# Performance work log

Hardware: AMD Instinct MI355X
Metric: run time of the kernel (lower is better)

Reference implementation:

```python
import jax, jax.numpy as jnp
import numpy as np

N_NODES = 100000
N_EDGES = 1600000
D_IN = 256
D_OUT = 128


def setup_inputs() -> dict:
    key = jax.random.key(0)
    k1, k2, k3, k4, k5, k6 = jax.random.split(key, 6)
    inp = {
        "input": jax.random.normal(k1, (N_NODES, D_IN), dtype=jnp.float32),
        "edge_row": jax.random.randint(k2, (N_EDGES,), 0, N_NODES),
        "edge_col": jax.random.randint(k3, (N_EDGES,), 0, N_NODES),
        "edge_val": jax.random.uniform(k4, (N_EDGES,), dtype=jnp.float32),
        "W": jax.random.normal(k5, (D_IN, D_OUT), dtype=jnp.float32) * (1.0 / np.sqrt(D_IN)),
        "b": jax.random.normal(k6, (D_OUT,), dtype=jnp.float32) * 0.01,
    }
    return inp


def reference(input, edge_row, edge_col, edge_val, W, b):
    # support = Linear(input)  -> [N, D_OUT]
    support = jnp.dot(input, W) + b
    # sparse.mm(adj, support): out[r] = sum_e val[e] * support[col[e]] for edges with row[e]==r
    msgs = edge_val[:, None] * support[edge_col]  # [E, D_OUT]
    agg = jax.ops.segment_sum(msgs, edge_row, num_segments=N_NODES)  # [N, D_OUT]
    return jnp.tanh(agg)
```

## Files before the change

kernel.cpp:

```cpp
#include <hip/hip_runtime.h>
#include <math.h>

#define N_NODES 100000
#define N_EDGES 1600000
#define D_IN 256
#define D_OUT 128

#define OFF_SUPPORT 0
#define OFF_COUNTS  51200000
#define OFF_CSREV   51600008
#define OFF_BSUMS   64400008
#define OFF_WTHI    64400416
#define OFF_WTLO    64465952

#define SCAN_CHUNK  1024
#define SCAN_BLOCKS ((N_NODES + SCAN_CHUNK - 1) / SCAN_CHUNK)

#define GB 128
#define GEMM_BLOCKS ((N_NODES + GB - 1) / GB)
#define EDGE_BLOCKS ((N_EDGES + 255) / 256)
#define WCONV_BLOCKS ((D_IN * D_OUT) / 256)

typedef __attribute__((ext_vector_type(8))) short s8v;
typedef __attribute__((ext_vector_type(4))) float f4v;

__device__ __forceinline__ short f2bf(float x) {
  unsigned u = __float_as_uint(x);
  unsigned r = u + 0x7FFF + ((u >> 16) & 1);
  return (short)(r >> 16);
}
__device__ __forceinline__ float bf2f(short h) {
  return __uint_as_float(((unsigned)(unsigned short)h) << 16);
}

__device__ __forceinline__ void cvt8(float4 a, float4 b, s8v& h, s8v& l) {
  float f[8] = {a.x, a.y, a.z, a.w, b.x, b.y, b.z, b.w};
#pragma unroll
  for (int i = 0; i < 8; i++) {
    short hh = f2bf(f[i]);
    h[i] = hh;
    l[i] = f2bf(f[i] - bf2f(hh));
  }
}

__device__ __forceinline__ void gload_lds16(const void* g, void* l) {
  __builtin_amdgcn_global_load_lds(
      (const __attribute__((address_space(1))) void*)g,
      (__attribute__((address_space(3))) void*)l, 16, 0, 0);
}

#define VMW(N)                                             \
  asm volatile("s_waitcnt vmcnt(" #N ")" ::: "memory");    \
  __builtin_amdgcn_sched_barrier(0)
#define SBAR()                    \
  __builtin_amdgcn_s_barrier();   \
  __builtin_amdgcn_sched_barrier(0)

__global__ __launch_bounds__(256) void prep_kernel(
    const float* __restrict__ W, short* __restrict__ wt_hi,
    short* __restrict__ wt_lo, const int* __restrict__ erow,
    int* __restrict__ counts, int* __restrict__ pos_e) {
  if (blockIdx.x < WCONV_BLOCKS) {
    int idx = blockIdx.x * 256 + threadIdx.x;
    int k = idx >> 7;
    int n = idx & 127;
    float v = W[idx];
    short h = f2bf(v);
    wt_hi[n * 256 + k] = h;
    wt_lo[n * 256 + k] = f2bf(v - bf2f(h));
  } else {
    int e = (blockIdx.x - WCONV_BLOCKS) * 256 + threadIdx.x;
    if (e < N_EDGES) pos_e[e] = atomicAdd(&counts[erow[e]], 1);
  }
}

__device__ __forceinline__ void gemm_body(
    int gb, const float* __restrict__ input, const short* __restrict__ wt_hi,
    const short* __restrict__ wt_lo, const float* __restrict__ b,
    float* __restrict__ support) {
  __shared__ short Bh[2][128][64];
  __shared__ short Bl[2][128][64];
  const int t = threadIdx.x;
  const int lane = t & 63;
  const int wv = t >> 6;
  const int qm = lane & 15;
  const int quad = lane >> 4;
  const int node0 = gb * GB;

  int r0 = node0 + wv * 32 + qm;
  int r1 = r0 + 16;
  if (r0 > N_NODES - 1) r0 = N_NODES - 1;
  if (r1 > N_NODES - 1) r1 = N_NODES - 1;
  const float* a0p = input + (size_t)r0 * D_IN + quad * 8;
  const float* a1p = input + (size_t)r1 * D_IN + quad * 8;

  const int lrow = lane >> 3;
  const int lpc = lane & 7;
  auto stageB = [&](int q, int p) {
    const int rb = wv * 32;
#pragma unroll
    for (int j = 0; j < 4; ++j) {
      int n = rb + j * 8 + lrow;
      int sc = lpc ^ (n & 7);
      const short* sh = wt_hi + (size_t)n * 256 + q * 64 + sc * 8;
      const short* sl = wt_lo + (size_t)n * 256 + q * 64 + sc * 8;
      gload_lds16(sh, &Bh[p][rb + j * 8][0]);
      gload_lds16(sl, &Bl[p][rb + j * 8][0]);
    }
  };

  float4 A0[4], A1[4], A2[4];
  auto loadA = [&](float4* d, int s) {
    d[0] = *(const float4*)(a0p + s * 32);
    d[1] = *(const float4*)(a0p + s * 32 + 4);
    d[2] = *(const float4*)(a1p + s * 32);
    d[3] = *(const float4*)(a1p + s * 32 + 4);
  };

  f4v acc[2][8];
#pragma unroll
  for (int mt = 0; mt < 2; mt++)
#pragma unroll
    for (int nt = 0; nt < 8; nt++) acc[mt][nt] = (f4v){0.f, 0.f, 0.f, 0.f};

  s8v ah0, al0, ah1, al1;
  auto cvtA = [&](const float4* X) {
    cvt8(X[0], X[1], ah0, al0);
    cvt8(X[2], X[3], ah1, al1);
  };
  auto mfma8 = [&](int p, int si) {
#pragma unroll
    for (int nt = 0; nt < 8; ++nt) {
      int n = nt * 16 + qm;
      int pc = (si * 4 + quad) ^ (n & 7);
      s8v bh = *(const s8v*)&Bh[p][n][pc * 8];
      s8v bl = *(const s8v*)&Bl[p][n][pc * 8];
      acc[0][nt] = __builtin_amdgcn_mfma_f32_16x16x32_bf16(ah0, bh, acc[0][nt], 0, 0, 0);
      acc[0][nt] = __builtin_amdgcn_mfma_f32_16x16x32_bf16(ah0, bl, acc[0][nt], 0, 0, 0);
      acc[0][nt] = __builtin_amdgcn_mfma_f32_16x16x32_bf16(al0, bh, acc[0][nt], 0, 0, 0);
      acc[1][nt] = __builtin_amdgcn_mfma_f32_16x16x32_bf16(ah1, bh, acc[1][nt], 0, 0, 0);
      acc[1][nt] = __builtin_amdgcn_mfma_f32_16x16x32_bf16(ah1, bl, acc[1][nt], 0, 0, 0);
      acc[1][nt] = __builtin_amdgcn_mfma_f32_16x16x32_bf16(al1, bh, acc[1][nt], 0, 0, 0);
    }
  };

  stageB(0, 0);
  loadA(A0, 0);
  loadA(A1, 1);
  loadA(A2, 2);
  VMW(8);
  SBAR();
  cvtA(A0);
  stageB(1, 1);
  loadA(A0, 3);
  mfma8(0, 0);
  VMW(16);
  cvtA(A1);
  loadA(A1, 4);
  mfma8(0, 1);
  VMW(8);
  SBAR();
  cvtA(A2);
  stageB(2, 0);
  loadA(A2, 5);
  mfma8(1, 0);
  VMW(16);
  cvtA(A0);
  loadA(A0, 6);
  mfma8(1, 1);
  VMW(8);
  SBAR();
  cvtA(A1);
  stageB(3, 1);
  loadA(A1, 7);
  mfma8(0, 0);
  VMW(16);
  cvtA(A2);
  mfma8(0, 1);
  VMW(4);
  SBAR();
  cvtA(A0);
  mfma8(1, 0);
  VMW(0);
  cvtA(A1);
  mfma8(1, 1);

  float bias[8];
#pragma unroll
  for (int nt = 0; nt < 8; nt++) bias[nt] = b[nt * 16 + qm];
#pragma unroll
  for (int mt = 0; mt < 2; mt++) {
#pragma unroll
    for (int nt = 0; nt < 8; nt++) {
      int col = nt * 16 + qm;
#pragma unroll
      for (int r = 0; r < 4; r++) {
        int node = node0 + wv * 32 + mt * 16 + quad * 4 + r;
        if (node < N_NODES)
          support[(size_t)node * D_OUT + col] = acc[mt][nt][r] + bias[nt];
      }
    }
  }
}

__global__ __launch_bounds__(256, 2) void gemm_build_kernel(
    const float* __restrict__ input, const short* __restrict__ wt_hi,
    const short* __restrict__ wt_lo, const float* __restrict__ b,
    float* __restrict__ support, const int* __restrict__ erow,
    const int* __restrict__ ecol, const float* __restrict__ eval,
    const int* __restrict__ offsets, const int* __restrict__ pos_e,
    long long* __restrict__ csr_ev) {
  if (blockIdx.x < GEMM_BLOCKS) {
    gemm_body(blockIdx.x, input, wt_hi, wt_lo, b, support);
  } else {
    int e = (blockIdx.x - GEMM_BLOCKS) * 256 + threadIdx.x;
    if (e < N_EDGES) {
      int r = __builtin_nontemporal_load(erow + e);
      int c = __builtin_nontemporal_load(ecol + e);
      int vb = __builtin_nontemporal_load((const int*)eval + e);
      int p = __builtin_nontemporal_load(pos_e + e);
      int idx = offsets[r] + p;
      long long packed = (unsigned int)c | ((long long)(unsigned int)vb << 32);
      csr_ev[idx] = packed;
    }
  }
}

__global__ __launch_bounds__(256) void scan_phase1(const int* __restrict__ counts,
                                                   int* __restrict__ bsums) {
  __shared__ int ts[256];
  int t = threadIdx.x;
  int idx0 = blockIdx.x * SCAN_CHUNK + t * 4;
  int s = 0;
#pragma unroll
  for (int i = 0; i < 4; i++)
    if (idx0 + i < N_NODES) s += counts[idx0 + i];
  ts[t] = s;
  __syncthreads();
#pragma unroll
  for (int off = 128; off > 0; off >>= 1) {
    if (t < off) ts[t] += ts[t + off];
    __syncthreads();
  }
  if (t == 0) bsums[blockIdx.x] = ts[0];
}

__global__ __launch_bounds__(128) void scan_phase2(int* __restrict__ bsums) {
  __shared__ int s[128];
  int t = threadIdx.x;
  int v = (t < SCAN_BLOCKS) ? bsums[t] : 0;
  s[t] = v;
  __syncthreads();
#pragma unroll
  for (int off = 1; off < 128; off <<= 1) {
    int x = (t >= off) ? s[t - off] : 0;
    __syncthreads();
    s[t] += x;
    __syncthreads();
  }
  if (t < SCAN_BLOCKS) bsums[t] = s[t] - v;
}

__global__ __launch_bounds__(256) void scan_phase3(int* __restrict__ counts,
                                                   const int* __restrict__ bsums) {
  __shared__ int ts[256];
  int t = threadIdx.x;
  int b = blockIdx.x;
  int idx0 = b * SCAN_CHUNK + t * 4;
  int v[4];
  int s = 0;
#pragma unroll
  for (int i = 0; i < 4; i++) {
    v[i] = (idx0 + i < N_NODES) ? counts[idx0 + i] : 0;
    s += v[i];
  }
  ts[t] = s;
  __syncthreads();
#pragma unroll
  for (int off = 1; off < 256; off <<= 1) {
    int x = (t >= off) ? ts[t - off] : 0;
    __syncthreads();
    ts[t] += x;
    __syncthreads();
  }
  int run = bsums[b] + ts[t] - s;
#pragma unroll
  for (int i = 0; i < 4; i++) {
    int idx = idx0 + i;
    if (idx < N_NODES) counts[idx] = run;
    run += v[i];
  }
  if (b == 0 && t == 0) counts[N_NODES] = N_EDGES;
}

__global__ __launch_bounds__(256) void agg_kernel(
    const int* __restrict__ offsets, const long long* __restrict__ csr_ev,
    const float* __restrict__ support, float* __restrict__ out) {
  int r = blockIdx.x * 8 + (threadIdx.x >> 5);
  int l4 = (threadIdx.x & 31) * 4;
  int beg = offsets[r];
  int end = offsets[r + 1];
  float4 acc = make_float4(0.f, 0.f, 0.f, 0.f);

  if (end > beg) {
    int ec[8], encol[8];
    float ev[8], env[8];
#pragma unroll
    for (int u = 0; u < 8; u++) {
      int idx = beg + u;
      int c = idx < end ? idx : end - 1;
      long long p = csr_ev[c];
      ec[u] = (int)(unsigned int)p;
      ev[u] = (idx < end) ? __uint_as_float((unsigned int)(p >> 32)) : 0.f;
    }
    for (int j = beg; j < end; j += 8) {
      int jn = j + 8;
      if (jn < end) {
#pragma unroll
        for (int u = 0; u < 8; u++) {
          int idx = jn + u;
          int c = idx < end ? idx : end - 1;
          long long p = csr_ev[c];
          encol[u] = (int)(unsigned int)p;
          env[u] = (idx < end) ? __uint_as_float((unsigned int)(p >> 32)) : 0.f;
        }
      }
      float4 s[8];
#pragma unroll
      for (int u = 0; u < 8; u++)
        s[u] = *(const float4*)(support + (size_t)ec[u] * D_OUT + l4);
#pragma unroll
      for (int u = 0; u < 8; u++) {
        acc.x = fmaf(ev[u], s[u].x, acc.x);
        acc.y = fmaf(ev[u], s[u].y, acc.y);
        acc.z = fmaf(ev[u], s[u].z, acc.z);
        acc.w = fmaf(ev[u], s[u].w, acc.w);
      }
#pragma unroll
      for (int u = 0; u < 8; u++) { ec[u] = encol[u]; ev[u] = env[u]; }
    }
  }
  *(float4*)(out + (size_t)r * D_OUT + l4) =
      make_float4(tanhf(acc.x), tanhf(acc.y), tanhf(acc.z), tanhf(acc.w));
}

extern "C" void kernel_launch(void* const* d_in, const int* in_sizes, int n_in,
                              void* d_out, int out_size, void* d_ws, size_t ws_size,
                              hipStream_t stream) {
  const float* input = (const float*)d_in[0];
  const int* erow = (const int*)d_in[1];
  const int* ecol = (const int*)d_in[2];
  const float* eval = (const float*)d_in[3];
  const float* W = (const float*)d_in[4];
  const float* b = (const float*)d_in[5];
  float* out = (float*)d_out;

  char* ws = (char*)d_ws;
  float* support = (float*)(ws + OFF_SUPPORT);
  int* counts = (int*)(ws + OFF_COUNTS);
  long long* csr_ev = (long long*)(ws + OFF_CSREV);
  int* bsums = (int*)(ws + OFF_BSUMS);
  short* wt_hi = (short*)(ws + OFF_WTHI);
  short* wt_lo = (short*)(ws + OFF_WTLO);
  int* pos_e = (int*)d_out;

  hipMemsetAsync(ws + OFF_COUNTS, 0, (size_t)(N_NODES + 1) * 4, stream);

  hipLaunchKernelGGL(prep_kernel, dim3(WCONV_BLOCKS + EDGE_BLOCKS), dim3(256),
                     0, stream, W, wt_hi, wt_lo, erow, counts, pos_e);
  hipLaunchKernelGGL(scan_phase1, dim3(SCAN_BLOCKS), dim3(256), 0, stream,
                     counts, bsums);
  hipLaunchKernelGGL(scan_phase2, dim3(1), dim3(128), 0, stream, bsums);
  hipLaunchKernelGGL(scan_phase3, dim3(SCAN_BLOCKS), dim3(256), 0, stream,
                     counts, bsums);
  hipLaunchKernelGGL(gemm_build_kernel, dim3(GEMM_BLOCKS + EDGE_BLOCKS),
                     dim3(256), 0, stream, input, wt_hi, wt_lo, b, support,
                     erow, ecol, eval, counts, pos_e, csr_ev);
  hipLaunchKernelGGL(agg_kernel, dim3(N_NODES / 8), dim3(256), 0, stream,
                     counts, csr_ev, support, out);
}
```

Before: 422.7 us.

## Replace three-phase scan with single-pass decoupled lookback scan and batch edge work

Merges the three scan kernels into one decoupled-lookback scan that publishes per-block aggregate and inclusive flags in a state array, which prep_kernel zeroes. This removes two kernel launches and the dependency gaps between them. The histogram and CSR-build edge blocks now process 8 edges per thread with loads batched ahead of atomics and scatters, to expose more memory-level parallelism. The lookback spin-waits on earlier blocks and relies on all 98 scan blocks making forward progress.

```diff
diff --git a/kernel.cpp b/kernel.cpp
--- a/kernel.cpp
+++ b/kernel.cpp
@@ -9,7 +9,7 @@
 #define OFF_SUPPORT 0
 #define OFF_COUNTS  51200000
 #define OFF_CSREV   51600008
-#define OFF_BSUMS   64400008
+#define OFF_STATE   64400008
 #define OFF_WTHI    64400416
 #define OFF_WTLO    64465952
 
@@ -18,8 +18,9 @@
 
 #define GB 128
 #define GEMM_BLOCKS ((N_NODES + GB - 1) / GB)
-#define EDGE_BLOCKS ((N_EDGES + 255) / 256)
 #define WCONV_BLOCKS ((D_IN * D_OUT) / 256)
+#define HIST_BLOCKS ((N_EDGES + 2047) / 2048)
+#define BUILD_BLOCKS ((N_EDGES + 2047) / 2048)
 
 typedef __attribute__((ext_vector_type(8))) short s8v;
 typedef __attribute__((ext_vector_type(4))) float f4v;
@@ -59,19 +60,94 @@
 __global__ __launch_bounds__(256) void prep_kernel(
     const float* __restrict__ W, short* __restrict__ wt_hi,
     short* __restrict__ wt_lo, const int* __restrict__ erow,
-    int* __restrict__ counts, int* __restrict__ pos_e) {
+    int* __restrict__ counts, int* __restrict__ pos_e,
+    unsigned* __restrict__ state) {
+  const int t = threadIdx.x;
   if (blockIdx.x < WCONV_BLOCKS) {
-    int idx = blockIdx.x * 256 + threadIdx.x;
+    int idx = blockIdx.x * 256 + t;
     int k = idx >> 7;
     int n = idx & 127;
     float v = W[idx];
     short h = f2bf(v);
     wt_hi[n * 256 + k] = h;
     wt_lo[n * 256 + k] = f2bf(v - bf2f(h));
+    if (blockIdx.x == 0 && t < SCAN_BLOCKS) state[t] = 0;
   } else {
-    int e = (blockIdx.x - WCONV_BLOCKS) * 256 + threadIdx.x;
-    if (e < N_EDGES) pos_e[e] = atomicAdd(&counts[erow[e]], 1);
-  }
+    int base = (blockIdx.x - WCONV_BLOCKS) * 2048 + t;
+    int r[8];
+#pragma unroll
+    for (int u = 0; u < 8; u++) {
+      int e = base + u * 256;
+      r[u] = (e < N_EDGES) ? erow[e] : -1;
+    }
+#pragma unroll
+    for (int u = 0; u < 8; u++) {
+      int e = base + u * 256;
+      if (r[u] >= 0) pos_e[e] = atomicAdd(&counts[r[u]], 1);
+    }
+  }
+}
+
+__global__ __launch_bounds__(256) void scan_kernel(
+    int* __restrict__ counts, unsigned* __restrict__ state) {
+  __shared__ int ts[256];
+  __shared__ int sprev;
+  const int t = threadIdx.x;
+  const int b = blockIdx.x;
+  int idx0 = b * SCAN_CHUNK + t * 4;
+  int v[4];
+  int s = 0;
+#pragma unroll
+  for (int i = 0; i < 4; i++) {
+    v[i] = (idx0 + i < N_NODES) ? counts[idx0 + i] : 0;
+    s += v[i];
+  }
+  ts[t] = s;
+  __syncthreads();
+#pragma unroll
+  for (int off = 1; off < 256; off <<= 1) {
+    int x = (t >= off) ? ts[t - off] : 0;
+    __syncthreads();
+    ts[t] += x;
+    __syncthreads();
+  }
+  int total = ts[255];
+  if (t == 0)
+    atomicExch(&state[b], ((unsigned)total << 2) | (b == 0 ? 2u : 1u));
+  if (b == 0) {
+    if (t == 0) sprev = 0;
+  } else if (t < 64) {
+    unsigned run = 0;
+    int look = b - 1;
+    for (;;) {
+      int p = look - t;
+      unsigned sv = 2u;
+      if (p >= 0) {
+        do { sv = atomicAdd(&state[p], 0u); } while ((sv & 3u) == 0u);
+      }
+      unsigned long long mask = __ballot((sv & 3u) == 2u);
+      int fl = (mask != 0ULL) ? (__ffsll((long long)mask) - 1) : 64;
+      unsigned c = (t <= fl) ? (sv >> 2) : 0u;
+#pragma unroll
+      for (int o = 32; o > 0; o >>= 1) c += __shfl_down(c, o);
+      if (t == 0) run += c;
+      if (mask != 0ULL) break;
+      look -= 64;
+    }
+    if (t == 0) {
+      sprev = (int)run;
+      atomicExch(&state[b], ((run + (unsigned)total) << 2) | 2u);
+    }
+  }
+  __syncthreads();
+  int run0 = sprev + ts[t] - s;
+#pragma unroll
+  for (int i = 0; i < 4; i++) {
+    int idx = idx0 + i;
+    if (idx < N_NODES) counts[idx] = run0;
+    run0 += v[i];
+  }
+  if (b == 0 && t == 0) counts[N_NODES] = N_EDGES;
 }
 
 __device__ __forceinline__ void gemm_body(
@@ -213,84 +289,32 @@
   if (blockIdx.x < GEMM_BLOCKS) {
     gemm_body(blockIdx.x, input, wt_hi, wt_lo, b, support);
   } else {
-    int e = (blockIdx.x - GEMM_BLOCKS) * 256 + threadIdx.x;
-    if (e < N_EDGES) {
-      int r = __builtin_nontemporal_load(erow + e);
-      int c = __builtin_nontemporal_load(ecol + e);
-      int vb = __builtin_nontemporal_load((const int*)eval + e);
-      int p = __builtin_nontemporal_load(pos_e + e);
-      int idx = offsets[r] + p;
-      long long packed = (unsigned int)c | ((long long)(unsigned int)vb << 32);
-      csr_ev[idx] = packed;
-    }
-  }
-}
-
-__global__ __launch_bounds__(256) void scan_phase1(const int* __restrict__ counts,
-                                                   int* __restrict__ bsums) {
-  __shared__ int ts[256];
-  int t = threadIdx.x;
-  int idx0 = blockIdx.x * SCAN_CHUNK + t * 4;
-  int s = 0;
-#pragma unroll
-  for (int i = 0; i < 4; i++)
-    if (idx0 + i < N_NODES) s += counts[idx0 + i];
-  ts[t] = s;
-  __syncthreads();
-#pragma unroll
-  for (int off = 128; off > 0; off >>= 1) {
-    if (t < off) ts[t] += ts[t + off];
-    __syncthreads();
-  }
-  if (t == 0) bsums[blockIdx.x] = ts[0];
-}
-
-__global__ __launch_bounds__(128) void scan_phase2(int* __restrict__ bsums) {
-  __shared__ int s[128];
-  int t = threadIdx.x;
-  int v = (t < SCAN_BLOCKS) ? bsums[t] : 0;
-  s[t] = v;
-  __syncthreads();
-#pragma unroll
-  for (int off = 1; off < 128; off <<= 1) {
-    int x = (t >= off) ? s[t - off] : 0;
-    __syncthreads();
-    s[t] += x;
-    __syncthreads();
-  }
-  if (t < SCAN_BLOCKS) bsums[t] = s[t] - v;
-}
-
-__global__ __launch_bounds__(256) void scan_phase3(int* __restrict__ counts,
-                                                   const int* __restrict__ bsums) {
-  __shared__ int ts[256];
-  int t = threadIdx.x;
-  int b = blockIdx.x;
-  int idx0 = b * SCAN_CHUNK + t * 4;
-  int v[4];
-  int s = 0;
-#pragma unroll
-  for (int i = 0; i < 4; i++) {
-    v[i] = (idx0 + i < N_NODES) ? counts[idx0 + i] : 0;
-    s += v[i];
-  }
-  ts[t] = s;
-  __syncthreads();
-#pragma unroll
-  for (int off = 1; off < 256; off <<= 1) {
-    int x = (t >= off) ? ts[t - off] : 0;
-    __syncthreads();
-    ts[t] += x;
-    __syncthreads();
-  }
-  int run = bsums[b] + ts[t] - s;
-#pragma unroll
-  for (int i = 0; i < 4; i++) {
-    int idx = idx0 + i;
-    if (idx < N_NODES) counts[idx] = run;
-    run += v[i];
-  }
-  if (b == 0 && t == 0) counts[N_NODES] = N_EDGES;
+    int base = (blockIdx.x - GEMM_BLOCKS) * 2048 + threadIdx.x;
+    int r[8], p[8];
+#pragma unroll
+    for (int u = 0; u < 8; u++) {
+      int e = base + u * 256;
+      bool ok = e < N_EDGES;
+      r[u] = ok ? __builtin_nontemporal_load(erow + e) : -1;
+      p[u] = ok ? __builtin_nontemporal_load(pos_e + e) : 0;
+    }
+    int off[8];
+#pragma unroll
+    for (int u = 0; u < 8; u++) off[u] = (r[u] >= 0) ? offsets[r[u]] : 0;
+    long long pk[8];
+#pragma unroll
+    for (int u = 0; u < 8; u++) {
+      int e = base + u * 256;
+      if (r[u] >= 0) {
+        int c = __builtin_nontemporal_load(ecol + e);
+        int vb = __builtin_nontemporal_load((const int*)eval + e);
+        pk[u] = (unsigned)c | ((long long)(unsigned)vb << 32);
+      }
+    }
+#pragma unroll
+    for (int u = 0; u < 8; u++)
+      if (r[u] >= 0) csr_ev[off[u] + p[u]] = pk[u];
+  }
 }
 
 __global__ __launch_bounds__(256) void agg_kernel(
@@ -359,21 +383,18 @@
   float* support = (float*)(ws + OFF_SUPPORT);
   int* counts = (int*)(ws + OFF_COUNTS);
   long long* csr_ev = (long long*)(ws + OFF_CSREV);
-  int* bsums = (int*)(ws + OFF_BSUMS);
+  unsigned* state = (unsigned*)(ws + OFF_STATE);
   short* wt_hi = (short*)(ws + OFF_WTHI);
   short* wt_lo = (short*)(ws + OFF_WTLO);
   int* pos_e = (int*)d_out;
 
   hipMemsetAsync(ws + OFF_COUNTS, 0, (size_t)(N_NODES + 1) * 4, stream);
 
-  hipLaunchKernelGGL(prep_kernel, dim3(WCONV_BLOCKS + EDGE_BLOCKS), dim3(256),
-                     0, stream, W, wt_hi, wt_lo, erow, counts, pos_e);
-  hipLaunchKernelGGL(scan_phase1, dim3(SCAN_BLOCKS), dim3(256), 0, stream,
-                     counts, bsums);
-  hipLaunchKernelGGL(scan_phase2, dim3(1), dim3(128), 0, stream, bsums);
-  hipLaunchKernelGGL(scan_phase3, dim3(SCAN_BLOCKS), dim3(256), 0, stream,
-                     counts, bsums);
-  hipLaunchKernelGGL(gemm_build_kernel, dim3(GEMM_BLOCKS + EDGE_BLOCKS),
+  hipLaunchKernelGGL(prep_kernel, dim3(WCONV_BLOCKS + HIST_BLOCKS), dim3(256),
+                     0, stream, W, wt_hi, wt_lo, erow, counts, pos_e, state);
+  hipLaunchKernelGGL(scan_kernel, dim3(SCAN_BLOCKS), dim3(256), 0, stream,
+                     counts, state);
+  hipLaunchKernelGGL(gemm_build_kernel, dim3(GEMM_BLOCKS + BUILD_BLOCKS),
                      dim3(256), 0, stream, input, wt_hi, wt_lo, b, support,
                      erow, ecol, eval, counts, pos_e, csr_ev);
   hipLaunchKernelGGL(agg_kernel, dim3(N_NODES / 8), dim3(256), 0, stream,
```

Measured after the change: 411.6 us. -2.6%, faster.
